# Kernel tuning notes

Hardware: AMD Instinct MI355X
Metric: run time of the kernel (lower is better)

The kernel has to match this reference:

```python
import jax, jax.numpy as jnp
import numpy as np

N_SAMPLES = 256   # n_samples from __init__
N_THIN = 10       # N from __init__
N_WORDS = 4096


def setup_inputs() -> dict:
    key = jax.random.key(0)
    k1, k2, k3 = jax.random.split(key, 3)
    # scale potentials so per-step weight deltas stay in a sane exp() range
    bigram = jax.random.normal(k1, (N_WORDS, N_WORDS), dtype=jnp.float32)
    start = jax.random.normal(k2, (N_WORDS,), dtype=jnp.float32)
    end = jax.random.normal(k3, (N_WORDS,), dtype=jnp.float32)
    return {"n_words": N_WORDS, "bigram": bigram, "start": start, "end": end}


def _mh_chain(bigram, start, end, n_words, chain_size, rng):
    # chain[0] = identity permutation (random_start=False)
    perm0 = jnp.arange(n_words, dtype=jnp.int32)
    w0 = bigram[perm0[:-1], perm0[1:]].sum() + start[perm0[0]] + end[perm0[-1]]

    def step(carry, k):
        perm, w_last = carry
        k_pos, k_cat, k_u = jax.random.split(k, 3)
        # pick a token to move, remove it -> perm2 of length n_words-1
        pos = jax.random.randint(k_pos, (), 0, n_words)
        to_move = perm[pos]
        j = jnp.arange(n_words - 1)
        perm2 = perm[j + (j >= pos).astype(j.dtype)]
        # insertion logits over n_words slots (self._probs, unnormalized log p)
        logits = jnp.zeros((n_words,), dtype=bigram.dtype)
        logits = logits.at[0].add(start[to_move]).at[-1].add(end[to_move])
        logits = logits.at[1:].add(bigram[perm2, to_move])   # left-neighbor term
        logits = logits.at[:-1].add(bigram[to_move, perm2])  # right-neighbor term
        p = jax.nn.softmax(logits)
        new_pos = jax.random.categorical(k_cat, logits)
        # insert to_move at new_pos
        jj = jnp.arange(n_words)
        shifted = perm2[jnp.clip(jj - (jj > new_pos).astype(jj.dtype), 0, n_words - 2)]
        sample = jnp.where(jj == new_pos, to_move, shifted).astype(perm.dtype)
        # new chain weight
        new_w = bigram[sample[:-1], sample[1:]].sum() + start[sample[0]] + end[sample[-1]]
        # MH accept ratio; removing to_move from sample recovers perm2, so the
        # reverse insertion distribution equals p -> ratio p[new_pos]/p[pos]
        acc = jnp.minimum(1.0, jnp.exp(new_w - w_last) * p[new_pos] / p[pos])
        accept = acc > jax.random.uniform(k_u, ())
        perm_next = jnp.where(accept, sample, perm)
        w_next = jnp.where(accept, new_w, w_last)
        return (perm_next, w_next), perm_next

    keys = jax.random.split(rng, chain_size - 1)
    _, perms = jax.lax.scan(step, (perm0, w0), keys)
    chain = jnp.concatenate([perm0[None, :], perms], axis=0)  # [chain_size, n_words]
    sel = jnp.arange(0, chain_size, N_THIN) + (N_THIN - 1)    # thin: every N-th state
    return chain[sel]


def reference(n_words, bigram, start, end):
    chain_size = N_SAMPLES * N_THIN
    rng = jax.random.key(42)
    return _mh_chain(bigram, start, end, n_words, chain_size, rng)
```

## Files before the change

kernel.cpp:

```cpp
#include <hip/hip_runtime.h>
#include <stdint.h>


#define NW 4096
#define NSTEPS 2559
#define NTHREADS 1024
#define NWAVES 16

typedef unsigned long long u64;
typedef uint32_t u32;
typedef unsigned short u16;

__device__ __forceinline__ u32 rotl32(u32 v, u32 r) { return (v << r) | (v >> (32u - r)); }

__device__ __forceinline__ void tf2x32(u32 k0, u32 k1, u32 x0, u32 x1, u32* o0, u32* o1) {
  u32 ks2 = k0 ^ k1 ^ 0x1BD11BDAu;
  x0 += k0; x1 += k1;
#define TFR(r0, r1, r2, r3)                      \
  x0 += x1; x1 = rotl32(x1, r0); x1 ^= x0;       \
  x0 += x1; x1 = rotl32(x1, r1); x1 ^= x0;       \
  x0 += x1; x1 = rotl32(x1, r2); x1 ^= x0;       \
  x0 += x1; x1 = rotl32(x1, r3); x1 ^= x0;
  TFR(13, 15, 26, 6)  x0 += k1;  x1 += ks2 + 1u;
  TFR(17, 29, 16, 24) x0 += ks2; x1 += k0 + 2u;
  TFR(13, 15, 26, 6)  x0 += k0;  x1 += k1 + 3u;
  TFR(17, 29, 16, 24) x0 += k1;  x1 += ks2 + 4u;
  TFR(13, 15, 26, 6)  x0 += ks2; x1 += k0 + 5u;
#undef TFR
  *o0 = x0; *o1 = x1;
}

__device__ __forceinline__ float unif01(u32 bits) {
  return __uint_as_float((bits >> 9) | 0x3f800000u) - 1.0f;
}

__device__ __forceinline__ u32 fkey(float f) {
  u32 b = __float_as_uint(f);
  return b ^ ((b >> 31) ? 0xFFFFFFFFu : 0x80000000u);
}


template <int CTRL>
__device__ __forceinline__ u32 dpp32(u32 v) {
  return (u32)__builtin_amdgcn_update_dpp(0, (int)v, CTRL, 0xF, 0xF, true);
}

template <int CTRL>
__device__ __forceinline__ void dppmax64(u32& hi, u32& lo) {
  u32 h2 = dpp32<CTRL>(hi);
  u32 l2 = dpp32<CTRL>(lo);
  bool g = (h2 > hi) || (h2 == hi && l2 > lo);
  hi = g ? h2 : hi;
  lo = g ? l2 : lo;
}

__device__ __forceinline__ u64 wave_max_u64(u64 key) {
  u32 lo = (u32)key, hi = (u32)(key >> 32);
  dppmax64<0x111>(hi, lo); dppmax64<0x112>(hi, lo);
  dppmax64<0x114>(hi, lo); dppmax64<0x118>(hi, lo);
  dppmax64<0x142>(hi, lo); dppmax64<0x143>(hi, lo);
  return ((u64)hi << 32) | lo;
}

__device__ __forceinline__ u64 bfly16_max_u64(u64 key) {
  u32 lo = (u32)key, hi = (u32)(key >> 32);
  dppmax64<0xB1>(hi, lo); dppmax64<0x4E>(hi, lo);
  dppmax64<0x141>(hi, lo); dppmax64<0x140>(hi, lo);
  return ((u64)hi << 32) | lo;
}


#define TT 32
__global__ void transpose_k(const float* __restrict__ in, float* __restrict__ out) {
  __shared__ float tile[TT][TT + 1];
  int x = blockIdx.x * TT + threadIdx.x;
  int y = blockIdx.y * TT + threadIdx.y;
  for (int j = 0; j < TT; j += 8) tile[threadIdx.y + j][threadIdx.x] = in[(u64)(y + j) * NW + x];
  __syncthreads();
  x = blockIdx.y * TT + threadIdx.x;
  y = blockIdx.x * TT + threadIdx.y;
  for (int j = 0; j < TT; j += 8) out[(u64)(y + j) * NW + x] = tile[threadIdx.x][threadIdx.y + j];
}

__global__ void gumbel_k(float* __restrict__ gumb) {
  long long idx = (long long)blockIdx.x * blockDim.x + threadIdx.x;
  if (idx >= (long long)NSTEPS * NW) return;
  int t = (int)(idx >> 12);
  int i = (int)(idx & (NW - 1));
  u32 kt0, kt1, kc0, kc1, ba, bb;
  tf2x32(0u, 42u, 0u, (u32)t, &kt0, &kt1);
  tf2x32(kt0, kt1, 0u, 1u, &kc0, &kc1);
  tf2x32(kc0, kc1, 0u, (u32)i, &ba, &bb);
  float u = unif01(ba ^ bb);
  if (u == 0.0f) u = 1.17549435e-38f;
  float t1 = (float)log((double)u);
  float t2 = (float)log((double)(-t1));
  gumb[idx] = -t2;
}

__global__ void posu_k(int* __restrict__ posArr, float* __restrict__ uArr) {
  int t = blockIdx.x * blockDim.x + threadIdx.x;
  if (t >= NSTEPS) return;
  u32 kt0, kt1, kp0, kp1, ku0, ku1, k2a, k2b, ra, rb, ua, ub;
  tf2x32(0u, 42u, 0u, (u32)t, &kt0, &kt1);
  tf2x32(kt0, kt1, 0u, 0u, &kp0, &kp1);
  tf2x32(kt0, kt1, 0u, 2u, &ku0, &ku1);
  tf2x32(kp0, kp1, 0u, 1u, &k2a, &k2b);
  tf2x32(k2a, k2b, 0u, 0u, &ra, &rb);
  posArr[t] = (int)((ra ^ rb) & (u32)(NW - 1));
  tf2x32(ku0, ku1, 0u, 0u, &ua, &ub);
  uArr[t] = unif01(ua ^ ub);
}


#define SAMPLE_AT(idx)                                                        \
  ((idx) < np ? (int)s_perm[(idx) + ((idx) >= pos)]                           \
              : ((idx) == np ? tm                                             \
                             : (int)s_perm[((idx)-1) + (((idx)-1) >= pos)]))

__global__ __launch_bounds__(NTHREADS)
void mcmc_fast11(const float* __restrict__ bigram,
                 const float* __restrict__ bigT,
                 const float* __restrict__ gumb,
                 const int* __restrict__ posArr,
                 const float* __restrict__ uArr,
                 const float* __restrict__ startv,
                 const float* __restrict__ endv,
                 int* __restrict__ out) {
  __shared__ u16    s_perm[NW];
  __shared__ float2 s_rows[NW];
  __shared__ u64    s_redu[NWAVES];
  __shared__ float  s_stm, s_etm, s_lpos;
  __shared__ int    s_accs;

  const int tid = threadIdx.x;
  const int lane = tid & 63;
  const int wid = tid >> 6;
  const int j0 = tid * 4;

  for (int i = tid; i < NW; i += NTHREADS) s_perm[i] = (u16)i;

  int pos = posArr[0];
  int tm = pos;
  {
    float4 rb4 = ((const float4*)(bigram + (u64)tm * NW))[tid];
    float4 rt4 = ((const float4*)(bigT + (u64)tm * NW))[tid];
    ((float4*)(&s_rows[j0]))[0] = make_float4(rt4.x, rb4.x, rt4.y, rb4.y);
    ((float4*)(&s_rows[j0]))[1] = make_float4(rt4.z, rb4.z, rt4.w, rb4.w);
  }
  if (tid == 0) { s_stm = startv[tm]; s_etm = endv[tm]; }

  float u_cur = uArr[0];
  float start_cur = startv[0];
  float end_cur = endv[NW - 1];
  float brg = 0.0f;
  if (pos >= 1 && pos <= NW - 2) brg = bigram[(u64)(pos - 1) * NW + (pos + 1)];

  float4 g4 = ((const float4*)gumb)[tid];
  __syncthreads();

  for (int t = 0; t < NSTEPS; ++t) {
    const float gg[4] = {g4.x, g4.y, g4.z, g4.w};
    int pos_nxt; float u_nxt;
    {
      int tn = (t + 1 < NSTEPS) ? (t + 1) : (NSTEPS - 1);
      g4 = ((const float4*)(gumb + ((u64)tn << 12)))[tid];
      pos_nxt = posArr[tn];
      u_nxt = uArr[tn];
    }
    ushort4 pq = ((const ushort4*)s_perm)[tid];
    const int p0i = pq.x, p1i = pq.y, p2i = pq.z, p3i = pq.w;
    int pm1, pp4;
    {
      u32 lo = (u32)pq.x | ((u32)pq.y << 16);
      u32 hi = (u32)pq.z | ((u32)pq.w << 16);
      pm1 = (int)(dpp32<0x138>(hi) >> 16);
      pp4 = (int)(dpp32<0x130>(lo) & 0xFFFFu);
      if (lane == 0)  pm1 = (tid > 0) ? (int)s_perm[j0 - 1] : 0;
      if (lane == 63) pp4 = (tid < NTHREADS - 1) ? (int)s_perm[j0 + 4] : 0;
    }
    const int w0 = (j0     >= pos) ? p1i : p0i;
    const int w1 = (j0 + 1 >= pos) ? p2i : p1i;
    const int w2 = (j0 + 2 >= pos) ? p3i : p2i;
    const int w3 = (j0 + 3 >= pos) ? pp4 : p3i;
    const int wprev = ((j0 - 1) >= pos) ? p0i : pm1;
    const float2 f0 = s_rows[w0];
    const float2 f1 = s_rows[w1];
    const float2 f2 = s_rows[w2];
    const float2 f3 = s_rows[w3];
    float tprev = __uint_as_float(dpp32<0x138>(__float_as_uint(f3.x)));
    if (lane == 0 && tid > 0) tprev = s_rows[wprev].x;
    float li0 = tprev + f0.y;
    float li1 = f0.x + f1.y;
    float li2 = f1.x + f2.y;
    float li3 = f2.x + f3.y;
    if (tid == 0)            li0 = s_stm + f0.y;
    if (tid == NTHREADS - 1) li3 = s_etm + f2.x;
    if ((pos >> 2) == tid) {
      int k = pos & 3;
      s_lpos = (k == 0) ? li0 : ((k == 1) ? li1 : ((k == 2) ? li2 : li3));
    }
    u64 best;
    {
      u64 b0 = ((u64)fkey(gg[0] + li0) << 32) | (u32)(NW - 1 - j0);
      u64 b1 = ((u64)fkey(gg[1] + li1) << 32) | (u32)(NW - 2 - j0);
      u64 b2 = ((u64)fkey(gg[2] + li2) << 32) | (u32)(NW - 3 - j0);
      u64 b3 = ((u64)fkey(gg[3] + li3) << 32) | (u32)(NW - 4 - j0);
      best = b0 > b1 ? b0 : b1;
      u64 b23 = b2 > b3 ? b2 : b3;
      if (b23 > best) best = b23;
    }
    best = wave_max_u64(best);
    if (lane == 63) s_redu[wid] = best;
    __syncthreads();

    int np;
    {
      u64 bb = bfly16_max_u64(s_redu[lane & 15]);
      np = NW - 1 - (int)(bb & 0xFFFFFFFFu);
    }
    const int tmR = (int)s_perm[pos_nxt];
    const int tmA = SAMPLE_AT(pos_nxt);
    ushort4 st;
    st.x = (j0     < np) ? (u16)w0 : ((j0     == np) ? (u16)tm : (u16)wprev);
    st.y = (j0 + 1 < np) ? (u16)w1 : ((j0 + 1 == np) ? (u16)tm : (u16)w0);
    st.z = (j0 + 2 < np) ? (u16)w2 : ((j0 + 2 == np) ? (u16)tm : (u16)w1);
    st.w = (j0 + 3 < np) ? (u16)w3 : ((j0 + 3 == np) ? (u16)tm : (u16)w2);
    int plA = 0, prA = 0, plR = 0, prR = 0;
    const bool ibn = (pos_nxt >= 1 && pos_nxt <= NW - 2);
    if (wid == 0) {
      int ls_i = (np >= 1) ? ((np - 1) + ((np - 1) >= pos)) : 0;
      int rs_i = (np <= NW - 2) ? (np + (np >= pos)) : 0;
      const int l_s = (int)s_perm[ls_i];
      const int r_s = (int)s_perm[rs_i];
      float splitv = bigram[(u64)l_s * NW + r_s];
      int s0 = (np > 0) ? (int)s_perm[(0 >= pos) ? 1 : 0] : tm;
      int sl = (np < NW - 1) ? (int)s_perm[(NW - 2) + ((NW - 2) >= pos)] : tm;
      float sv0 = startv[s0];
      float ev1 = endv[sl];
      float remL = 0.0f, remR = 0.0f;
      if (pos > 0)      remL = s_rows[s_perm[pos - 1]].x;
      if (pos < NW - 1) remR = s_rows[s_perm[pos + 1]].y;
      float vnpm1 = (np >= 1)      ? s_rows[l_s].x : 0.0f;
      float vnp   = (np <= NW - 2) ? s_rows[r_s].y : 0.0f;
      if (ibn) {
        plR = (int)s_perm[pos_nxt - 1]; prR = (int)s_perm[pos_nxt + 1];
        plA = SAMPLE_AT(pos_nxt - 1);   prA = SAMPLE_AT(pos_nxt + 1);
      }
      float stm_r = s_stm, etm_r = s_etm;
      float lposv = s_lpos;
      double delta = 0.0;
      if (pos > 0)                 delta -= (double)remL;
      if (pos < NW - 1)            delta -= (double)remR;
      if (pos > 0 && pos < NW - 1) delta += (double)brg;
      if (np > 0)                  delta += (double)vnpm1;
      if (np < NW - 1)             delta += (double)vnp;
      if (np > 0 && np < NW - 1)   delta -= (double)splitv;
      delta += ((double)sv0 - (double)start_cur) + ((double)ev1 - (double)end_cur);
      float lnp = (np == 0) ? (stm_r + vnp)
                : ((np == NW - 1) ? (etm_r + vnpm1) : (vnpm1 + vnp));
      double ed = delta + ((double)lnp - (double)lposv);
      float a = fminf(1.0f, expf((float)ed));
      int acc = (a > u_cur) ? 1 : 0;
      if (lane == 0) s_accs = acc;
      if (acc) { start_cur = sv0; end_cur = ev1; }
    }
    __syncthreads();

    const int acc = s_accs;
    const int tm_next = acc ? tmA : tmR;
    const float4 rb4 = ((const float4*)(bigram + (u64)tm_next * NW))[tid];
    const float4 rt4 = ((const float4*)(bigT + (u64)tm_next * NW))[tid];
    if (wid == 0) {
      float stmN = startv[tm_next];
      float etmN = endv[tm_next];
      brg = 0.0f;
      if (ibn) {
        int pl = acc ? plA : plR;
        int pr = acc ? prA : prR;
        brg = bigram[(u64)pl * NW + pr];
      }
      if (lane == 0) { s_stm = stmN; s_etm = etmN; }
    }
    if (acc) ((ushort4*)s_perm)[tid] = st;
    ((float4*)(&s_rows[j0]))[0] = make_float4(rt4.x, rb4.x, rt4.y, rb4.y);
    ((float4*)(&s_rows[j0]))[1] = make_float4(rt4.z, rb4.z, rt4.w, rb4.w);
    tm = tm_next;
    pos = pos_nxt;
    u_cur = u_nxt;
    __syncthreads();

    if ((t % 10) == 8) {
      int row = (t - 8) / 10;
      ushort4 p4 = ((const ushort4*)s_perm)[tid];
      int4 o4;
      o4.x = (int)p4.x; o4.y = (int)p4.y; o4.z = (int)p4.z; o4.w = (int)p4.w;
      ((int4*)(out + (u64)row * NW))[tid] = o4;
    }
  }
}


__global__ __launch_bounds__(NTHREADS)
void mcmc_kernel(const float* __restrict__ bigram,
                 const float* __restrict__ startv,
                 const float* __restrict__ endv,
                 int* __restrict__ out) {
  __shared__ int    s_perm[NW];
  __shared__ float  s_logit[NW];
  __shared__ float  s_gath[NW];
  __shared__ float  s_redf[NWAVES];
  __shared__ u64    s_redu[NWAVES];
  __shared__ double s_redd[NWAVES];
  __shared__ float  s_m, s_Z, s_w;
  __shared__ int    s_pos, s_tm, s_np, s_acc;
  __shared__ u32    s_kcat0, s_kcat1, s_ku0, s_ku1;

  const int tid = threadIdx.x;
  const int lane = tid & 63;
  const int wid = tid >> 6;

  for (int i = tid; i < NW; i += NTHREADS) s_perm[i] = i;
  for (int j = tid; j < NW - 1; j += NTHREADS) s_gath[j] = bigram[(u64)j * NW + (j + 1)];
  __syncthreads();
  if (tid == 0) {
    float S = 0.0f;
    for (int j = 0; j < NW - 1; ++j) S += s_gath[j];
    S = S + startv[0];
    S = S + endv[NW - 1];
    s_w = S;
  }
  __syncthreads();

  for (int t = 0; t < NSTEPS; ++t) {
    if (tid == 0) {
      u32 kt0, kt1;
      tf2x32(0u, 42u, 0u, (u32)t, &kt0, &kt1);
      u32 kp0, kp1, kc0, kc1, ku0, ku1;
      tf2x32(kt0, kt1, 0u, 0u, &kp0, &kp1);
      tf2x32(kt0, kt1, 0u, 1u, &kc0, &kc1);
      tf2x32(kt0, kt1, 0u, 2u, &ku0, &ku1);
      u32 k2a, k2b, ra, rb;
      tf2x32(kp0, kp1, 0u, 1u, &k2a, &k2b);
      tf2x32(k2a, k2b, 0u, 0u, &ra, &rb);
      int pos = (int)((ra ^ rb) & (u32)(NW - 1));
      s_pos = pos;
      s_tm = s_perm[pos];
      s_kcat0 = kc0; s_kcat1 = kc1; s_ku0 = ku0; s_ku1 = ku1;
    }
    __syncthreads();
    const int pos = s_pos, tm = s_tm;

    float lmax = -3.402823466e+38f;
    for (int i = tid; i < NW; i += NTHREADS) {
      float li;
      if (i == 0) {
        int r = s_perm[(0 >= pos) ? 1 : 0];
        li = startv[tm] + bigram[(u64)tm * NW + r];
      } else if (i == NW - 1) {
        int l = s_perm[((NW - 2) >= pos) ? (NW - 1) : (NW - 2)];
        li = endv[tm] + bigram[(u64)l * NW + tm];
      } else {
        int l = s_perm[((i - 1) >= pos) ? i : (i - 1)];
        int r = s_perm[(i >= pos) ? (i + 1) : i];
        li = bigram[(u64)l * NW + tm] + bigram[(u64)tm * NW + r];
      }
      s_logit[i] = li;
      lmax = fmaxf(lmax, li);
    }
    for (int o = 32; o > 0; o >>= 1) lmax = fmaxf(lmax, __shfl_down(lmax, o, 64));
    if (lane == 0) s_redf[wid] = lmax;
    __syncthreads();
    if (tid == 0) {
      float m = s_redf[0];
      for (int w = 1; w < NWAVES; ++w) m = fmaxf(m, s_redf[w]);
      s_m = m;
    }
    __syncthreads();
    const float m = s_m;

    double zacc = 0.0;
    u64 best = 0;
    const u32 kc0 = s_kcat0, kc1 = s_kcat1;
    for (int i = tid; i < NW; i += NTHREADS) {
      float li = s_logit[i];
      float ex = (float)exp((double)(li - m));
      zacc += (double)ex;
      u32 ba, bb;
      tf2x32(kc0, kc1, 0u, (u32)i, &ba, &bb);
      float u = unif01(ba ^ bb);
      if (u == 0.0f) u = 1.17549435e-38f;
      float t1 = (float)log((double)u);
      float t2 = (float)log((double)(-t1));
      float g = -t2;
      float sv = g + li;
      u64 key = ((u64)fkey(sv) << 32) | (u32)(NW - 1 - i);
      if (key > best) best = key;
    }
    for (int o = 32; o > 0; o >>= 1) {
      u64 w = __shfl_down(best, o, 64);
      if (w > best) best = w;
      zacc += __shfl_down(zacc, o, 64);
    }
    if (lane == 0) { s_redu[wid] = best; s_redd[wid] = zacc; }
    __syncthreads();
    if (tid == 0) {
      u64 b = s_redu[0]; double z = s_redd[0];
      for (int w = 1; w < NWAVES; ++w) {
        if (s_redu[w] > b) b = s_redu[w];
        z += s_redd[w];
      }
      s_np = NW - 1 - (int)(b & 0xFFFFFFFFu);
      s_Z = (float)z;
    }
    __syncthreads();
    const int np = s_np;

    for (int j = tid; j < NW - 1; j += NTHREADS) {
      int a = (j < np) ? s_perm[j + (j >= pos)]
                       : ((j == np) ? tm : s_perm[(j - 1) + ((j - 1) >= pos)]);
      int j1 = j + 1;
      int b = (j1 < np) ? s_perm[j1 + (j1 >= pos)]
                        : ((j1 == np) ? tm : s_perm[(j1 - 1) + ((j1 - 1) >= pos)]);
      s_gath[j] = bigram[(u64)a * NW + b];
    }
    __syncthreads();

    if (tid == 0) {
      float S = 0.0f;
      for (int j = 0; j < NW - 1; ++j) S += s_gath[j];
      int s0 = (0 < np) ? s_perm[(0 >= pos) ? 1 : 0] : tm;
      int sl = ((NW - 1) == np) ? tm : s_perm[(NW - 2) + ((NW - 2) >= pos)];
      S = S + startv[s0];
      S = S + endv[sl];
      float dw = S - s_w;
      float e1 = (float)exp((double)dw);
      float en = (float)exp((double)(s_logit[np] - m));
      float eo = (float)exp((double)(s_logit[pos] - m));
      float pn = en / s_Z;
      float po = eo / s_Z;
      float acc = e1 * pn;
      acc = acc / po;
      acc = fminf(1.0f, acc);
      u32 ua, ub;
      tf2x32(s_ku0, s_ku1, 0u, 0u, &ua, &ub);
      float u = unif01(ua ^ ub);
      int accept = (acc > u) ? 1 : 0;
      s_acc = accept;
      if (accept) s_w = S;
    }
    __syncthreads();

    int stash[4];
    if (s_acc) {
      for (int k = 0; k < 4; ++k) {
        int i = tid + k * NTHREADS;
        stash[k] = (i < np) ? s_perm[i + (i >= pos)]
                            : ((i == np) ? tm : s_perm[(i - 1) + ((i - 1) >= pos)]);
      }
    }
    __syncthreads();
    if (s_acc) {
      for (int k = 0; k < 4; ++k) {
        int i = tid + k * NTHREADS;
        s_perm[i] = stash[k];
      }
    }
    __syncthreads();

    if (((t + 1) % 10) == 9) {
      int row = (t - 8) / 10;
      for (int i = tid; i < NW; i += NTHREADS) out[(u64)row * NW + i] = s_perm[i];
    }
    __syncthreads();
  }
}

extern "C" void kernel_launch(void* const* d_in, const int* in_sizes, int n_in,
                              void* d_out, int out_size, void* d_ws, size_t ws_size,
                              hipStream_t stream) {
  const float* bigram = (const float*)d_in[1];
  const float* startv = (const float*)d_in[2];
  const float* endv   = (const float*)d_in[3];
  int* out = (int*)d_out;

  const size_t needT = (size_t)NW * NW * sizeof(float);
  const size_t needG = (size_t)NSTEPS * NW * sizeof(float);
  const size_t needP = (size_t)NSTEPS * (sizeof(int) + sizeof(float));

  if (ws_size >= needT + needG + needP) {
    float* bigT = (float*)d_ws;
    float* gumb = (float*)((char*)d_ws + needT);
    int* posArr = (int*)((char*)d_ws + needT + needG);
    float* uArr = (float*)((char*)d_ws + needT + needG + (size_t)NSTEPS * sizeof(int));
    hipLaunchKernelGGL(transpose_k, dim3(NW / TT, NW / TT), dim3(TT, 8), 0, stream,
                       bigram, bigT);
    long long ng = (long long)NSTEPS * NW;
    hipLaunchKernelGGL(gumbel_k, dim3((unsigned)((ng + 255) / 256)), dim3(256), 0, stream,
                       gumb);
    hipLaunchKernelGGL(posu_k, dim3((NSTEPS + 255) / 256), dim3(256), 0, stream,
                       posArr, uArr);
    hipLaunchKernelGGL(mcmc_fast11, dim3(1), dim3(NTHREADS), 0, stream,
                       bigram, bigT, gumb, posArr, uArr, startv, endv, out);
  } else {
    hipLaunchKernelGGL(mcmc_kernel, dim3(1), dim3(NTHREADS), 0, stream,
                       bigram, startv, endv, out);
  }
}
```

Measured before the change: 6.689 ms.

## Speculatively prefetch reject-path rows and cache adjacent-pair weights in LDS

Adds a shared-memory array holding the bigram weight of each adjacent pair in the current permutation, updated on acceptance, so the split and bridge weights come from LDS instead of dependent global gathers. The row of the token to move under rejection is loaded at the top of each step, overlapping the argmax reduction, and is refetched only when the proposal is accepted. The bridge gather now happens early in the step, off the critical path after the barrier. This shortens the serial dependency chain per MCMC step, at the cost of extra LDS, more select logic and a duplicate global row load on acceptance.

```diff
diff --git a/kernel.cpp b/kernel.cpp
--- a/kernel.cpp
+++ b/kernel.cpp
@@ -119,7 +119,7 @@
                              : (int)s_perm[((idx)-1) + (((idx)-1) >= pos)]))
 
 __global__ __launch_bounds__(NTHREADS)
-void mcmc_fast11(const float* __restrict__ bigram,
+void mcmc_fast12(const float* __restrict__ bigram,
                  const float* __restrict__ bigT,
                  const float* __restrict__ gumb,
                  const int* __restrict__ posArr,
@@ -129,8 +129,9 @@
                  int* __restrict__ out) {
   __shared__ u16    s_perm[NW];
   __shared__ float2 s_rows[NW];
+  __shared__ float  s_pairw[NW];
   __shared__ u64    s_redu[NWAVES];
-  __shared__ float  s_stm, s_etm, s_lpos;
+  __shared__ float  s_stm, s_etm, s_lpos, s_brgS, s_vn1, s_vn2;
   __shared__ int    s_accs;
 
   const int tid = threadIdx.x;
@@ -139,6 +140,11 @@
   const int j0 = tid * 4;
 
   for (int i = tid; i < NW; i += NTHREADS) s_perm[i] = (u16)i;
+#pragma unroll
+  for (int k = 0; k < 4; ++k) {
+    int j = j0 + k;
+    s_pairw[j] = (j < NW - 1) ? bigram[(u64)j * NW + (j + 1)] : 0.0f;
+  }
 
   int pos = posArr[0];
   int tm = pos;
@@ -153,8 +159,6 @@
   float u_cur = uArr[0];
   float start_cur = startv[0];
   float end_cur = endv[NW - 1];
-  float brg = 0.0f;
-  if (pos >= 1 && pos <= NW - 2) brg = bigram[(u64)(pos - 1) * NW + (pos + 1)];
 
   float4 g4 = ((const float4*)gumb)[tid];
   __syncthreads();
@@ -168,6 +172,12 @@
       pos_nxt = posArr[tn];
       u_nxt = uArr[tn];
     }
+    const int tmR = (int)s_perm[pos_nxt];
+    const float4 rbR = ((const float4*)(bigram + (u64)tmR * NW))[tid];
+    const float4 rtR = ((const float4*)(bigT + (u64)tmR * NW))[tid];
+    float stmR = 0.0f, etmR = 0.0f;
+    if (tid == 0) { stmR = startv[tmR]; etmR = endv[tmR]; }
+
     ushort4 pq = ((const ushort4*)s_perm)[tid];
     const int p0i = pq.x, p1i = pq.y, p2i = pq.z, p3i = pq.w;
     int pm1, pp4;
@@ -179,6 +189,29 @@
       if (lane == 0)  pm1 = (tid > 0) ? (int)s_perm[j0 - 1] : 0;
       if (lane == 63) pp4 = (tid < NTHREADS - 1) ? (int)s_perm[j0 + 4] : 0;
     }
+    float4 pwq = ((const float4*)s_pairw)[tid];
+    float pwm1, pwp4;
+    {
+      pwm1 = __uint_as_float(dpp32<0x138>(__float_as_uint(pwq.w)));
+      pwp4 = __uint_as_float(dpp32<0x130>(__float_as_uint(pwq.x)));
+      if (lane == 0)  pwm1 = (tid > 0) ? s_pairw[j0 - 1] : 0.0f;
+      if (lane == 63) pwp4 = (tid < NTHREADS - 1) ? s_pairw[j0 + 4] : 0.0f;
+    }
+
+    float stm_r = 0.0f, etm_r = 0.0f, remL = 0.0f, remR = 0.0f, brgv = 0.0f;
+    float sv0m = 0.0f, ev1m = 0.0f;
+    if (wid == 0) {
+      stm_r = s_stm; etm_r = s_etm;
+      int pl = (pos > 0) ? (int)s_perm[pos - 1] : 0;
+      int pr = (pos < NW - 1) ? (int)s_perm[pos + 1] : 0;
+      if (pos > 0)      remL = s_rows[pl].x;
+      if (pos < NW - 1) remR = s_rows[pr].y;
+      if (pos > 0 && pos < NW - 1) brgv = bigram[(u64)pl * NW + pr];
+      sv0m = startv[(int)s_perm[(0 >= pos) ? 1 : 0]];
+      ev1m = endv[(int)s_perm[(NW - 2) + ((NW - 2) >= pos)]];
+      if (lane == 0) s_brgS = brgv;
+    }
+
     const int w0 = (j0     >= pos) ? p1i : p0i;
     const int w1 = (j0 + 1 >= pos) ? p2i : p1i;
     const int w2 = (j0 + 2 >= pos) ? p3i : p2i;
@@ -219,40 +252,58 @@
       u64 bb = bfly16_max_u64(s_redu[lane & 15]);
       np = NW - 1 - (int)(bb & 0xFFFFFFFFu);
     }
-    const int tmR = (int)s_perm[pos_nxt];
     const int tmA = SAMPLE_AT(pos_nxt);
     ushort4 st;
     st.x = (j0     < np) ? (u16)w0 : ((j0     == np) ? (u16)tm : (u16)wprev);
     st.y = (j0 + 1 < np) ? (u16)w1 : ((j0 + 1 == np) ? (u16)tm : (u16)w0);
     st.z = (j0 + 2 < np) ? (u16)w2 : ((j0 + 2 == np) ? (u16)tm : (u16)w1);
     st.w = (j0 + 3 < np) ? (u16)w3 : ((j0 + 3 == np) ? (u16)tm : (u16)w2);
-    int plA = 0, prA = 0, plR = 0, prR = 0;
-    const bool ibn = (pos_nxt >= 1 && pos_nxt <= NW - 2);
+    const float brgAll = s_brgS;
+    float nv0, nv1, nv2, nv3;
+    {
+      float vA0 = (j0     < pos - 1) ? pwq.x : pwq.y;
+      float vB0 = (j0 - 1 < pos - 1) ? pwm1  : pwq.x;
+      nv0 = (j0 < np) ? vA0 : vB0;
+      int kk0 = (j0 < np) ? j0 : j0 - 1;
+      if (kk0 == pos - 1) nv0 = brgAll;
+
+      float vA1 = (j0 + 1 < pos - 1) ? pwq.y : pwq.z;
+      float vB1 = (j0     < pos - 1) ? pwq.x : pwq.y;
+      nv1 = (j0 + 1 < np) ? vA1 : vB1;
+      int kk1 = (j0 + 1 < np) ? j0 + 1 : j0;
+      if (kk1 == pos - 1) nv1 = brgAll;
+
+      float vA2 = (j0 + 2 < pos - 1) ? pwq.z : pwq.w;
+      float vB2 = (j0 + 1 < pos - 1) ? pwq.y : pwq.z;
+      nv2 = (j0 + 2 < np) ? vA2 : vB2;
+      int kk2 = (j0 + 2 < np) ? j0 + 2 : j0 + 1;
+      if (kk2 == pos - 1) nv2 = brgAll;
+
+      float vA3 = (j0 + 3 < pos - 1) ? pwq.w : pwp4;
+      float vB3 = (j0 + 2 < pos - 1) ? pwq.z : pwq.w;
+      nv3 = (j0 + 3 < np) ? vA3 : vB3;
+      int kk3 = (j0 + 3 < np) ? j0 + 3 : j0 + 2;
+      if (kk3 == pos - 1) nv3 = brgAll;
+    }
     if (wid == 0) {
       int ls_i = (np >= 1) ? ((np - 1) + ((np - 1) >= pos)) : 0;
       int rs_i = (np <= NW - 2) ? (np + (np >= pos)) : 0;
       const int l_s = (int)s_perm[ls_i];
       const int r_s = (int)s_perm[rs_i];
-      float splitv = bigram[(u64)l_s * NW + r_s];
-      int s0 = (np > 0) ? (int)s_perm[(0 >= pos) ? 1 : 0] : tm;
-      int sl = (np < NW - 1) ? (int)s_perm[(NW - 2) + ((NW - 2) >= pos)] : tm;
-      float sv0 = startv[s0];
-      float ev1 = endv[sl];
-      float remL = 0.0f, remR = 0.0f;
-      if (pos > 0)      remL = s_rows[s_perm[pos - 1]].x;
-      if (pos < NW - 1) remR = s_rows[s_perm[pos + 1]].y;
       float vnpm1 = (np >= 1)      ? s_rows[l_s].x : 0.0f;
       float vnp   = (np <= NW - 2) ? s_rows[r_s].y : 0.0f;
-      if (ibn) {
-        plR = (int)s_perm[pos_nxt - 1]; prR = (int)s_perm[pos_nxt + 1];
-        plA = SAMPLE_AT(pos_nxt - 1);   prA = SAMPLE_AT(pos_nxt + 1);
+      float splitv = 0.0f;
+      if (np > 0 && np < NW - 1) {
+        int k_s = (np - 1) + ((np - 1) >= pos);
+        splitv = (np == pos) ? brgv : s_pairw[k_s];
       }
-      float stm_r = s_stm, etm_r = s_etm;
+      float sv0 = (np > 0) ? sv0m : stm_r;
+      float ev1 = (np < NW - 1) ? ev1m : etm_r;
       float lposv = s_lpos;
       double delta = 0.0;
       if (pos > 0)                 delta -= (double)remL;
       if (pos < NW - 1)            delta -= (double)remR;
-      if (pos > 0 && pos < NW - 1) delta += (double)brg;
+      if (pos > 0 && pos < NW - 1) delta += (double)brgv;
       if (np > 0)                  delta += (double)vnpm1;
       if (np < NW - 1)             delta += (double)vnp;
       if (np > 0 && np < NW - 1)   delta -= (double)splitv;
@@ -262,29 +313,34 @@
       double ed = delta + ((double)lnp - (double)lposv);
       float a = fminf(1.0f, expf((float)ed));
       int acc = (a > u_cur) ? 1 : 0;
-      if (lane == 0) s_accs = acc;
+      if (lane == 0) { s_accs = acc; s_vn1 = vnpm1; s_vn2 = vnp; }
       if (acc) { start_cur = sv0; end_cur = ev1; }
     }
     __syncthreads();
 
     const int acc = s_accs;
     const int tm_next = acc ? tmA : tmR;
-    const float4 rb4 = ((const float4*)(bigram + (u64)tm_next * NW))[tid];
-    const float4 rt4 = ((const float4*)(bigT + (u64)tm_next * NW))[tid];
-    if (wid == 0) {
-      float stmN = startv[tm_next];
-      float etmN = endv[tm_next];
-      brg = 0.0f;
-      if (ibn) {
-        int pl = acc ? plA : plR;
-        int pr = acc ? prA : prR;
-        brg = bigram[(u64)pl * NW + pr];
-      }
-      if (lane == 0) { s_stm = stmN; s_etm = etmN; }
-    }
-    if (acc) ((ushort4*)s_perm)[tid] = st;
-    ((float4*)(&s_rows[j0]))[0] = make_float4(rt4.x, rb4.x, rt4.y, rb4.y);
-    ((float4*)(&s_rows[j0]))[1] = make_float4(rt4.z, rb4.z, rt4.w, rb4.w);
+    float4 rb = rbR, rt = rtR;
+    if (acc) {
+      rb = ((const float4*)(bigram + (u64)tm_next * NW))[tid];
+      rt = ((const float4*)(bigT + (u64)tm_next * NW))[tid];
+    }
+    if (tid == 0) {
+      s_stm = acc ? startv[tm_next] : stmR;
+      s_etm = acc ? endv[tm_next] : etmR;
+    }
+    if (acc) {
+      ((ushort4*)s_perm)[tid] = st;
+      float vn1 = s_vn1, vn2 = s_vn2;
+      float o0 = (j0     == np - 1) ? vn1 : ((j0     == np) ? vn2 : nv0);
+      float o1 = (j0 + 1 == np - 1) ? vn1 : ((j0 + 1 == np) ? vn2 : nv1);
+      float o2 = (j0 + 2 == np - 1) ? vn1 : ((j0 + 2 == np) ? vn2 : nv2);
+      float o3 = (j0 + 3 == np - 1) ? vn1 : ((j0 + 3 == np) ? vn2 : nv3);
+      if (j0 + 3 >= NW - 1) o3 = 0.0f;
+      ((float4*)s_pairw)[tid] = make_float4(o0, o1, o2, o3);
+    }
+    ((float4*)(&s_rows[j0]))[0] = make_float4(rt.x, rb.x, rt.y, rb.y);
+    ((float4*)(&s_rows[j0]))[1] = make_float4(rt.z, rb.z, rt.w, rb.w);
     tm = tm_next;
     pos = pos_nxt;
     u_cur = u_nxt;
@@ -500,7 +556,7 @@
                        gumb);
     hipLaunchKernelGGL(posu_k, dim3((NSTEPS + 255) / 256), dim3(256), 0, stream,
                        posArr, uArr);
-    hipLaunchKernelGGL(mcmc_fast11, dim3(1), dim3(NTHREADS), 0, stream,
+    hipLaunchKernelGGL(mcmc_fast12, dim3(1), dim3(NTHREADS), 0, stream,
                        bigram, bigT, gumb, posArr, uArr, startv, endv, out);
   } else {
     hipLaunchKernelGGL(mcmc_kernel, dim3(1), dim3(NTHREADS), 0, stream,
```

Measured after the change: 7.056 ms. 5.5% more time.
